# Performance work log

Hardware: AMD Instinct MI355X
Metric: run time of the kernel (lower is better)

The kernel has to match this reference:

```python
import jax, jax.numpy as jnp
import numpy as np

B, S, D_MODEL, HEADS = 2, 2048, 1024, 16
HEAD_DIM = D_MODEL // HEADS
NEG = -1.0e9


def setup_inputs() -> dict:
    key = jax.random.key(0)
    ks = jax.random.split(key, 7)
    query = jax.random.normal(ks[0], (B, S, D_MODEL), dtype=jnp.float32)
    k_in = jax.random.normal(ks[1], (B, S, D_MODEL), dtype=jnp.float32)
    value = jax.random.normal(ks[2], (B, S, D_MODEL), dtype=jnp.float32)
    # nn.Linear(d_model, d_model, bias=False) weights, torch layout [out, in]
    sc = 1.0 / np.sqrt(D_MODEL)
    Wq = jax.random.uniform(ks[3], (D_MODEL, D_MODEL), jnp.float32, -sc, sc)
    Wk = jax.random.uniform(ks[4], (D_MODEL, D_MODEL), jnp.float32, -sc, sc)
    Wv = jax.random.uniform(ks[5], (D_MODEL, D_MODEL), jnp.float32, -sc, sc)
    Wo = jax.random.uniform(ks[6], (D_MODEL, D_MODEL), jnp.float32, -sc, sc)
    # causal mask: 1 where attention allowed, 0 where masked
    mask = jnp.tril(jnp.ones((S, S), dtype=jnp.int32))[None, None]
    freqs_complex_form = jnp.zeros((1,), dtype=jnp.float32)  # unused by the module
    return {"query": query, "key": k_in, "value": value,
            "freqs_complex_form": freqs_complex_form, "mask": mask,
            "Wq": Wq, "Wk": Wk, "Wv": Wv, "Wo": Wo}


def reference(query, key, value, freqs_complex_form, mask, Wq, Wk, Wv, Wo):
    # QKV projections (torch Linear: y = x @ W.T)
    q = query @ Wq.T
    k = key @ Wk.T
    v = value @ Wv.T
    # [B, S, D] -> [B, H, S, Dh]
    q = q.reshape(B, S, HEADS, HEAD_DIM).transpose(0, 2, 1, 3)
    k = k.reshape(B, S, HEADS, HEAD_DIM).transpose(0, 2, 1, 3)
    v = v.reshape(B, S, HEADS, HEAD_DIM).transpose(0, 2, 1, 3)
    # scores [B, H, S, S]
    att = jnp.einsum('bhqd,bhkd->bhqk', q, k) / jnp.sqrt(jnp.float32(HEAD_DIM))
    att = jnp.where(mask == 0, NEG, att)
    att = jax.nn.softmax(att, axis=-1)
    # dropout is identity in eval / deterministic reference
    out = jnp.einsum('bhqk,bhkd->bhqd', att, v)
    out = out.transpose(0, 2, 1, 3).reshape(B, S, D_MODEL)
    return out @ Wo.T
```

## Files before the change

### kernel.cpp

```cpp
#include <hip/hip_runtime.h>

#define DM   1024
#define SEQ  2048
#define BATCH 2
#define NH   16
#define DHEAD 64
#define MTOT (BATCH*SEQ)
#define KVB  64

typedef _Float16 half_t;
typedef _Float16 half8 __attribute__((ext_vector_type(8)));
typedef float    floatx4 __attribute__((ext_vector_type(4)));

#define SCALE2 0.18033688f

__device__ __forceinline__ float fast_exp2(float x) {
  float r;
  asm volatile("v_exp_f32 %0, %1" : "=v"(r) : "v"(x));
  return r;
}

__device__ __forceinline__ void gload_lds16(const half_t* g, half_t* l) {
  __builtin_amdgcn_global_load_lds(
      (const __attribute__((address_space(1))) void*)g,
      (__attribute__((address_space(3))) void*)l, 16, 0, 0);
}

__global__ __launch_bounds__(256) void cvt_all(const float* __restrict__ q, const float* __restrict__ k,
                                               const float* __restrict__ v, const float* __restrict__ wq,
                                               const float* __restrict__ wk, const float* __restrict__ wv,
                                               const float* __restrict__ wo,
                                               half_t* __restrict__ dq, half_t* __restrict__ dk,
                                               half_t* __restrict__ dv, half_t* __restrict__ dwq,
                                               half_t* __restrict__ dwk, half_t* __restrict__ dwv,
                                               half_t* __restrict__ dwo) {
  const int y = blockIdx.y;
  const float* s; half_t* d; int n8;
  const int En8 = MTOT * DM / 8, Wn8 = DM * DM / 8;
  switch (y) {
    case 0: s = q;  d = dq;  n8 = En8; break;
    case 1: s = k;  d = dk;  n8 = En8; break;
    case 2: s = v;  d = dv;  n8 = En8; break;
    case 3: s = wq; d = dwq; n8 = Wn8; break;
    case 4: s = wk; d = dwk; n8 = Wn8; break;
    case 5: s = wv; d = dwv; n8 = Wn8; break;
    default: s = wo; d = dwo; n8 = Wn8; break;
  }
  int i = blockIdx.x * 256 + threadIdx.x;
  if (i >= n8) return;
  const float4* sp = reinterpret_cast<const float4*>(s);
  float4 u = sp[(size_t)i * 2], w = sp[(size_t)i * 2 + 1];
  half8 h;
  h[0] = (half_t)u.x; h[1] = (half_t)u.y; h[2] = (half_t)u.z; h[3] = (half_t)u.w;
  h[4] = (half_t)w.x; h[5] = (half_t)w.y; h[6] = (half_t)w.z; h[7] = (half_t)w.w;
  *reinterpret_cast<half8*>(d + (size_t)i * 8) = h;
}


#define GEMM_BODY(Ag, Bg, ...)                                                  \
  __shared__ half_t As[2][128 * 32];                                            \
  __shared__ half_t Bs[2][128 * 32];                                            \
  const int tid = threadIdx.x, lane = tid & 63, w = tid >> 6;                   \
  const int lr = lane & 15, lg = lane >> 4;                                     \
  const int swz = (flat & 7) * 32 + (flat >> 3);                                \
  const int m0 = (swz & 31) * 128, n0 = (swz >> 5) * 128;                       \
  const int wm = (w >> 1) * 64, wn = (w & 1) * 64;                              \
  floatx4 acc[4][4] = {};                                                       \
   \
  _Pragma("unroll")                                                             \
  for (int j = 0; j < 2; j++) {                                                 \
    int id = tid + j * 256;                                                     \
    gload_lds16(Ag + (size_t)(m0 + (id >> 2)) * DM + (id & 3) * 8,              \
                &As[0][id * 8]);                                                \
    gload_lds16(Bg + (size_t)(n0 + (id >> 2)) * DM + (id & 3) * 8,              \
                &Bs[0][id * 8]);                                                \
  }                                                                             \
  __syncthreads();                                                              \
  int buf = 0;                                                                  \
  _Pragma("unroll 1")                                                           \
  for (int t = 0; t < 31; t++) {                                                \
    const int k0 = (t + 1) * 32;                                                \
    _Pragma("unroll")                                                           \
    for (int j = 0; j < 2; j++) {                                               \
      int id = tid + j * 256;                                                   \
      gload_lds16(Ag + (size_t)(m0 + (id >> 2)) * DM + k0 + (id & 3) * 8,       \
                  &As[buf ^ 1][id * 8]);                                        \
      gload_lds16(Bg + (size_t)(n0 + (id >> 2)) * DM + k0 + (id & 3) * 8,       \
                  &Bs[buf ^ 1][id * 8]);                                        \
    }                                                                           \
    {                                                                           \
      half8 a[4], b[4];                                                         \
      _Pragma("unroll")                                                         \
      for (int i = 0; i < 4; i++)                                               \
        a[i] = *reinterpret_cast<half8*>(&As[buf][(wm + i * 16 + lr) * 32 + lg * 8]); \
      _Pragma("unroll")                                                         \
      for (int j = 0; j < 4; j++)                                               \
        b[j] = *reinterpret_cast<half8*>(&Bs[buf][(wn + j * 16 + lr) * 32 + lg * 8]); \
      _Pragma("unroll")                                                         \
      for (int i = 0; i < 4; i++)                                               \
        _Pragma("unroll")                                                       \
        for (int j = 0; j < 4; j++)                                             \
          acc[i][j] = __builtin_amdgcn_mfma_f32_16x16x32_f16(a[i], b[j],        \
                                                             acc[i][j], 0, 0, 0); \
    }                                                                           \
    __syncthreads();                                                            \
    buf ^= 1;                                                                   \
  }                                                                             \
  {                                                                             \
    half8 a[4], b[4];                                                           \
    _Pragma("unroll")                                                           \
    for (int i = 0; i < 4; i++)                                                 \
      a[i] = *reinterpret_cast<half8*>(&As[buf][(wm + i * 16 + lr) * 32 + lg * 8]); \
    _Pragma("unroll")                                                           \
    for (int j = 0; j < 4; j++)                                                 \
      b[j] = *reinterpret_cast<half8*>(&Bs[buf][(wn + j * 16 + lr) * 32 + lg * 8]); \
    _Pragma("unroll")                                                           \
    for (int i = 0; i < 4; i++)                                                 \
      _Pragma("unroll")                                                         \
      for (int j = 0; j < 4; j++)                                               \
        acc[i][j] = __builtin_amdgcn_mfma_f32_16x16x32_f16(a[i], b[j],          \
                                                           acc[i][j], 0, 0, 0); \
  }                                                                             \
  _Pragma("unroll")                                                             \
  for (int i = 0; i < 4; i++)                                                   \
    _Pragma("unroll")                                                           \
    for (int j = 0; j < 4; j++)                                                 \
      _Pragma("unroll")                                                         \
      for (int r = 0; r < 4; r++) {                                             \
        int m = m0 + wm + i * 16 + lg * 4 + r;                                  \
        int n = n0 + wn + j * 16 + lr;                                          \
        float v = acc[i][j][r];                                                 \
        __VA_ARGS__                                                             \
      }

__global__ __launch_bounds__(256) void gemm_qkv(const half_t* __restrict__ Xq,
                                                const half_t* __restrict__ Xk,
                                                const half_t* __restrict__ Xv,
                                                const half_t* __restrict__ Wq,
                                                const half_t* __restrict__ Wk,
                                                const half_t* __restrict__ Wv,
                                                half_t* __restrict__ Qb,
                                                half_t* __restrict__ Kb,
                                                half_t* __restrict__ Vb) {
  const int which = blockIdx.x >> 8;
  const int flat = blockIdx.x & 255;
  const half_t* Ag = (which == 0) ? Xq : (which == 1) ? Xk : Xv;
  const half_t* Bg = (which == 0) ? Wq : (which == 1) ? Wk : Wv;
  half_t* Cg       = (which == 0) ? Qb : (which == 1) ? Kb : Vb;
  const float esc  = (which == 0) ? SCALE2 : 1.0f;
  GEMM_BODY(Ag, Bg,
    int b_ = m >> 11;
    int s_ = m & 2047;
    int h_ = n >> 6;
    int d_ = n & 63;
    Cg[(((size_t)b_ * NH + h_) * SEQ + s_) * DHEAD + d_] = (half_t)(v * esc);)
}

__global__ __launch_bounds__(256) void gemm_o(const half_t* __restrict__ Ag,
                                              const half_t* __restrict__ Bg,
                                              float* __restrict__ Cg) {
  const int flat = blockIdx.x;
  GEMM_BODY(Ag, Bg, Cg[(size_t)m * DM + n] = v;)
}

__global__ __launch_bounds__(256) void attn_fwd(const half_t* __restrict__ Q,
                                                const half_t* __restrict__ K,
                                                const half_t* __restrict__ V,
                                                half_t* __restrict__ O) {
  __shared__ half_t Ks[64][72];
  __shared__ half_t Vt[80][72];
  __shared__ half_t Ps[4][16][72];
  const int tid = threadIdx.x, lane = tid & 63, w = tid >> 6;
  const int lr = lane & 15, lg = lane >> 4;

  const int flat = blockIdx.x;
  const int xcd = flat & 7, idx = flat >> 3;
  const int qblk = 31 - (idx >> 2);
  const int combo = xcd * 4 + (idx & 3);
  const int h = combo & 15, b = combo >> 4;

  const size_t bh = ((size_t)b * NH + h) * SEQ * DHEAD;
  const int q0 = qblk * 64 + w * 16;
  const int nt = qblk + 1;

  for (int i2 = tid; i2 < 16 * 72; i2 += 256) {
    int d = i2 / 72, kv = i2 % 72;
    Vt[64 + d][kv] = (d == 0) ? (half_t)1.0f : (half_t)0.0f;
  }

  half8 qf[2];
#pragma unroll
  for (int ks = 0; ks < 2; ks++)
    qf[ks] = *reinterpret_cast<const half8*>(
        Q + bh + (size_t)(q0 + lr) * DHEAD + ks * 32 + lg * 8);

  floatx4 accO[5] = {};

  half8 kr[2], vr[2];
#define LOADT(t)                                                              \
  {                                                                           \
    const int kvb2 = (t) * KVB;                                               \
    _Pragma("unroll")                                                         \
    for (int it = 0; it < 2; it++) {                                          \
      int c = tid + it * 256;                                                 \
      kr[it] = *reinterpret_cast<const half8*>(                               \
          K + bh + (size_t)(kvb2 + (c >> 3)) * DHEAD + (c & 7) * 8);          \
      vr[it] = *reinterpret_cast<const half8*>(                               \
          V + bh + (size_t)(kvb2 + (c & 63)) * DHEAD + (c >> 6) * 8);         \
    }                                                                         \
  }
#define WRITET()                                                              \
  {                                                                           \
    _Pragma("unroll")                                                         \
    for (int it = 0; it < 2; it++) {                                          \
      int c = tid + it * 256;                                                 \
      *reinterpret_cast<half8*>(&Ks[c >> 3][(c & 7) * 8]) = kr[it];           \
      int vrow = c & 63, vcol = (c >> 6) * 8;                                 \
      _Pragma("unroll")                                                       \
      for (int e = 0; e < 8; e++) Vt[vcol + e][vrow] = vr[it][e];             \
    }                                                                         \
  }

  LOADT(0);
  WRITET();
  __syncthreads();

#pragma unroll 1
  for (int t = 0; t < nt; t++) {
    const int kvbase = t * KVB;
    if (t + 1 < nt) LOADT(t + 1);
    const bool need_mask = (t == qblk);
    {
      floatx4 s[4];
#pragma unroll
      for (int jt = 0; jt < 4; jt++) {
        floatx4 a0 = {};
#pragma unroll
        for (int ks = 0; ks < 2; ks++) {
          half8 bk = *reinterpret_cast<half8*>(&Ks[jt * 16 + lr][ks * 32 + lg * 8]);
          a0 = __builtin_amdgcn_mfma_f32_16x16x32_f16(qf[ks], bk, a0, 0, 0, 0);
        }
        s[jt] = a0;
      }
#pragma unroll
      for (int r = 0; r < 4; r++) {
        const int q = q0 + lg * 4 + r;
#pragma unroll
        for (int jt = 0; jt < 4; jt++) {
          float pp = fast_exp2(s[jt][r]);
          if (need_mask) { int kv = kvbase + jt * 16 + lr; if (kv > q) pp = 0.f; }
          Ps[w][lg * 4 + r][jt * 16 + lr] = (half_t)pp;
        }
      }
#pragma unroll
      for (int j = 0; j < 5; j++) {
#pragma unroll
        for (int ks = 0; ks < 2; ks++) {
          half8 ap = *reinterpret_cast<half8*>(&Ps[w][lr][ks * 32 + lg * 8]);
          half8 bv = *reinterpret_cast<half8*>(&Vt[j * 16 + lr][ks * 32 + lg * 8]);
          accO[j] = __builtin_amdgcn_mfma_f32_16x16x32_f16(ap, bv, accO[j], 0, 0, 0);
        }
      }
    }
    if (t + 1 < nt) {
      __syncthreads();
      WRITET();
      __syncthreads();
    }
  }

#pragma unroll
  for (int r = 0; r < 4; r++) {
    float lsum = __shfl(accO[4][r], lane & 48);
    float inv = 1.0f / lsum;
    int q = q0 + lg * 4 + r;
#pragma unroll
    for (int j = 0; j < 4; j++) {
      float v = accO[j][r] * inv;
      O[((size_t)b * SEQ + q) * DM + h * DHEAD + j * 16 + lr] = (half_t)v;
    }
  }
#undef LOADT
#undef WRITET
}

extern "C" void kernel_launch(void* const* d_in, const int* in_sizes, int n_in,
                              void* d_out, int out_size, void* d_ws, size_t ws_size,
                              hipStream_t stream) {
  const float* q_in = (const float*)d_in[0];
  const float* k_in = (const float*)d_in[1];
  const float* v_in = (const float*)d_in[2];
  const float* Wq   = (const float*)d_in[5];
  const float* Wk   = (const float*)d_in[6];
  const float* Wv   = (const float*)d_in[7];
  const float* Wo   = (const float*)d_in[8];

  const size_t E = (size_t)MTOT * DM;
  const size_t W = (size_t)DM * DM;
  half_t* ws  = (half_t*)d_ws;
  half_t* Xq  = ws;
  half_t* Xk  = ws + E;
  half_t* Xv  = ws + 2 * E;
  half_t* Wqh = ws + 3 * E;
  half_t* Wkh = Wqh + W;
  half_t* Wvh = Wkh + W;
  half_t* Woh = Wvh + W;
  half_t* Qb  = ws + 4 * E;
  half_t* Kb  = ws + 5 * E;
  half_t* Vb  = ws + 6 * E;
  half_t* Ab  = Xq;
  if (ws_size < 7 * E * sizeof(half_t)) return;

  cvt_all<<<dim3(2048, 7), 256, 0, stream>>>(q_in, k_in, v_in, Wq, Wk, Wv, Wo,
                                             Xq, Xk, Xv, Wqh, Wkh, Wvh, Woh);
  gemm_qkv<<<768, 256, 0, stream>>>(Xq, Xk, Xv, Wqh, Wkh, Wvh, Qb, Kb, Vb);
  attn_fwd<<<1024, 256, 0, stream>>>(Qb, Kb, Vb, Ab);
  gemm_o<<<256, 256, 0, stream>>>(Ab, Woh, (float*)d_out);
}
```

Measured before the change: 141.1 us.

## Split attention KV range in two with a combine pass, narrow output GEMM tiles

The attention kernel now launches twice as many blocks. Each block handles half of the causal KV tiles for its query block and writes an unnormalized partial output plus a row-sum. A new combine kernel adds the two partials, normalizes them, and writes the head-interleaved activation. This is meant to improve load balance and occupancy across the triangular causal work, at the cost of an extra kernel and extra global traffic for the partial buffers. The output projection GEMM also switches to 128x64 tiles with 512 blocks, giving more parallelism on the smaller GEMM. The shared GEMM macro is replaced by explicit per-kernel code.

```diff
diff --git a/kernel.cpp b/kernel.cpp
--- a/kernel.cpp
+++ b/kernel.cpp
@@ -7,6 +7,8 @@
 #define DHEAD 64
 #define MTOT (BATCH*SEQ)
 #define KVB  64
+#define EOFF ((size_t)MTOT * DM)
+#define NROW (BATCH * NH * SEQ)
 
 typedef _Float16 half_t;
 typedef _Float16 half8 __attribute__((ext_vector_type(8)));
@@ -56,83 +58,6 @@
   *reinterpret_cast<half8*>(d + (size_t)i * 8) = h;
 }
 
-
-#define GEMM_BODY(Ag, Bg, ...)                                                  \
-  __shared__ half_t As[2][128 * 32];                                            \
-  __shared__ half_t Bs[2][128 * 32];                                            \
-  const int tid = threadIdx.x, lane = tid & 63, w = tid >> 6;                   \
-  const int lr = lane & 15, lg = lane >> 4;                                     \
-  const int swz = (flat & 7) * 32 + (flat >> 3);                                \
-  const int m0 = (swz & 31) * 128, n0 = (swz >> 5) * 128;                       \
-  const int wm = (w >> 1) * 64, wn = (w & 1) * 64;                              \
-  floatx4 acc[4][4] = {};                                                       \
-   \
-  _Pragma("unroll")                                                             \
-  for (int j = 0; j < 2; j++) {                                                 \
-    int id = tid + j * 256;                                                     \
-    gload_lds16(Ag + (size_t)(m0 + (id >> 2)) * DM + (id & 3) * 8,              \
-                &As[0][id * 8]);                                                \
-    gload_lds16(Bg + (size_t)(n0 + (id >> 2)) * DM + (id & 3) * 8,              \
-                &Bs[0][id * 8]);                                                \
-  }                                                                             \
-  __syncthreads();                                                              \
-  int buf = 0;                                                                  \
-  _Pragma("unroll 1")                                                           \
-  for (int t = 0; t < 31; t++) {                                                \
-    const int k0 = (t + 1) * 32;                                                \
-    _Pragma("unroll")                                                           \
-    for (int j = 0; j < 2; j++) {                                               \
-      int id = tid + j * 256;                                                   \
-      gload_lds16(Ag + (size_t)(m0 + (id >> 2)) * DM + k0 + (id & 3) * 8,       \
-                  &As[buf ^ 1][id * 8]);                                        \
-      gload_lds16(Bg + (size_t)(n0 + (id >> 2)) * DM + k0 + (id & 3) * 8,       \
-                  &Bs[buf ^ 1][id * 8]);                                        \
-    }                                                                           \
-    {                                                                           \
-      half8 a[4], b[4];                                                         \
-      _Pragma("unroll")                                                         \
-      for (int i = 0; i < 4; i++)                                               \
-        a[i] = *reinterpret_cast<half8*>(&As[buf][(wm + i * 16 + lr) * 32 + lg * 8]); \
-      _Pragma("unroll")                                                         \
-      for (int j = 0; j < 4; j++)                                               \
-        b[j] = *reinterpret_cast<half8*>(&Bs[buf][(wn + j * 16 + lr) * 32 + lg * 8]); \
-      _Pragma("unroll")                                                         \
-      for (int i = 0; i < 4; i++)                                               \
-        _Pragma("unroll")                                                       \
-        for (int j = 0; j < 4; j++)                                             \
-          acc[i][j] = __builtin_amdgcn_mfma_f32_16x16x32_f16(a[i], b[j],        \
-                                                             acc[i][j], 0, 0, 0); \
-    }                                                                           \
-    __syncthreads();                                                            \
-    buf ^= 1;                                                                   \
-  }                                                                             \
-  {                                                                             \
-    half8 a[4], b[4];                                                           \
-    _Pragma("unroll")                                                           \
-    for (int i = 0; i < 4; i++)                                                 \
-      a[i] = *reinterpret_cast<half8*>(&As[buf][(wm + i * 16 + lr) * 32 + lg * 8]); \
-    _Pragma("unroll")                                                           \
-    for (int j = 0; j < 4; j++)                                                 \
-      b[j] = *reinterpret_cast<half8*>(&Bs[buf][(wn + j * 16 + lr) * 32 + lg * 8]); \
-    _Pragma("unroll")                                                           \
-    for (int i = 0; i < 4; i++)                                                 \
-      _Pragma("unroll")                                                         \
-      for (int j = 0; j < 4; j++)                                               \
-        acc[i][j] = __builtin_amdgcn_mfma_f32_16x16x32_f16(a[i], b[j],          \
-                                                           acc[i][j], 0, 0, 0); \
-  }                                                                             \
-  _Pragma("unroll")                                                             \
-  for (int i = 0; i < 4; i++)                                                   \
-    _Pragma("unroll")                                                           \
-    for (int j = 0; j < 4; j++)                                                 \
-      _Pragma("unroll")                                                         \
-      for (int r = 0; r < 4; r++) {                                             \
-        int m = m0 + wm + i * 16 + lg * 4 + r;                                  \
-        int n = n0 + wn + j * 16 + lr;                                          \
-        float v = acc[i][j][r];                                                 \
-        __VA_ARGS__                                                             \
-      }
-
 __global__ __launch_bounds__(256) void gemm_qkv(const half_t* __restrict__ Xq,
                                                 const half_t* __restrict__ Xk,
                                                 const half_t* __restrict__ Xv,
@@ -142,31 +67,147 @@
                                                 half_t* __restrict__ Qb,
                                                 half_t* __restrict__ Kb,
                                                 half_t* __restrict__ Vb) {
+  __shared__ half_t As[2][128 * 32];
+  __shared__ half_t Bs[2][128 * 32];
   const int which = blockIdx.x >> 8;
   const int flat = blockIdx.x & 255;
   const half_t* Ag = (which == 0) ? Xq : (which == 1) ? Xk : Xv;
   const half_t* Bg = (which == 0) ? Wq : (which == 1) ? Wk : Wv;
   half_t* Cg       = (which == 0) ? Qb : (which == 1) ? Kb : Vb;
   const float esc  = (which == 0) ? SCALE2 : 1.0f;
-  GEMM_BODY(Ag, Bg,
-    int b_ = m >> 11;
-    int s_ = m & 2047;
-    int h_ = n >> 6;
-    int d_ = n & 63;
-    Cg[(((size_t)b_ * NH + h_) * SEQ + s_) * DHEAD + d_] = (half_t)(v * esc);)
+
+  const int tid = threadIdx.x, lane = tid & 63, w = tid >> 6;
+  const int lr = lane & 15, lg = lane >> 4;
+  const int swz = (flat & 7) * 32 + (flat >> 3);
+  const int m0 = (swz & 31) * 128, n0 = (swz >> 5) * 128;
+  const int wm = (w >> 1) * 64, wn = (w & 1) * 64;
+  floatx4 acc[4][4] = {};
+
+#define STAGE_QKV(BUF, K0)                                                    \
+  {                                                                           \
+    _Pragma("unroll")                                                         \
+    for (int j = 0; j < 2; j++) {                                             \
+      int id = tid + j * 256;                                                 \
+      gload_lds16(Ag + (size_t)(m0 + (id >> 2)) * DM + (K0) + (id & 3) * 8,   \
+                  &As[BUF][id * 8]);                                          \
+      gload_lds16(Bg + (size_t)(n0 + (id >> 2)) * DM + (K0) + (id & 3) * 8,   \
+                  &Bs[BUF][id * 8]);                                          \
+    }                                                                         \
+  }
+#define COMP_QKV(BUF)                                                         \
+  {                                                                           \
+    half8 a[4], b[4];                                                         \
+    _Pragma("unroll")                                                         \
+    for (int i = 0; i < 4; i++)                                               \
+      a[i] = *reinterpret_cast<half8*>(&As[BUF][(wm + i * 16 + lr) * 32 + lg * 8]); \
+    _Pragma("unroll")                                                         \
+    for (int j = 0; j < 4; j++)                                               \
+      b[j] = *reinterpret_cast<half8*>(&Bs[BUF][(wn + j * 16 + lr) * 32 + lg * 8]); \
+    _Pragma("unroll")                                                         \
+    for (int i = 0; i < 4; i++)                                               \
+      _Pragma("unroll")                                                       \
+      for (int j = 0; j < 4; j++)                                             \
+        acc[i][j] = __builtin_amdgcn_mfma_f32_16x16x32_f16(a[i], b[j], acc[i][j], 0, 0, 0); \
+  }
+
+  STAGE_QKV(0, 0);
+  __syncthreads();
+  int buf = 0;
+#pragma unroll 1
+  for (int t = 0; t < 31; t++) {
+    STAGE_QKV(buf ^ 1, (t + 1) * 32);
+    COMP_QKV(buf);
+    __syncthreads();
+    buf ^= 1;
+  }
+  COMP_QKV(buf);
+
+#pragma unroll
+  for (int i = 0; i < 4; i++)
+#pragma unroll
+    for (int j = 0; j < 4; j++)
+#pragma unroll
+      for (int r = 0; r < 4; r++) {
+        int m = m0 + wm + i * 16 + lg * 4 + r;
+        int n = n0 + wn + j * 16 + lr;
+        int b_ = m >> 11, s_ = m & 2047, h_ = n >> 6, d_ = n & 63;
+        Cg[(((size_t)b_ * NH + h_) * SEQ + s_) * DHEAD + d_] = (half_t)(acc[i][j][r] * esc);
+      }
+#undef STAGE_QKV
+#undef COMP_QKV
 }
 
 __global__ __launch_bounds__(256) void gemm_o(const half_t* __restrict__ Ag,
                                               const half_t* __restrict__ Bg,
                                               float* __restrict__ Cg) {
+  __shared__ half_t As[2][128 * 32];
+  __shared__ half_t Bs[2][64 * 32];
+  const int tid = threadIdx.x, lane = tid & 63, w = tid >> 6;
+  const int lr = lane & 15, lg = lane >> 4;
   const int flat = blockIdx.x;
-  GEMM_BODY(Ag, Bg, Cg[(size_t)m * DM + n] = v;)
+  const int swz = (flat & 7) * 64 + (flat >> 3);
+  const int m0 = (swz & 31) * 128, n0 = (swz >> 5) * 64;
+  const int wm = (w >> 1) * 64, wn = (w & 1) * 32;
+  floatx4 acc[4][2] = {};
+
+#define STAGE_O(BUF, K0)                                                      \
+  {                                                                           \
+    _Pragma("unroll")                                                         \
+    for (int j = 0; j < 2; j++) {                                             \
+      int id = tid + j * 256;                                                 \
+      gload_lds16(Ag + (size_t)(m0 + (id >> 2)) * DM + (K0) + (id & 3) * 8,   \
+                  &As[BUF][id * 8]);                                          \
+    }                                                                         \
+    gload_lds16(Bg + (size_t)(n0 + (tid >> 2)) * DM + (K0) + (tid & 3) * 8,   \
+                &Bs[BUF][tid * 8]);                                           \
+  }
+#define COMP_O(BUF)                                                           \
+  {                                                                           \
+    half8 a[4], b[2];                                                         \
+    _Pragma("unroll")                                                         \
+    for (int i = 0; i < 4; i++)                                               \
+      a[i] = *reinterpret_cast<half8*>(&As[BUF][(wm + i * 16 + lr) * 32 + lg * 8]); \
+    _Pragma("unroll")                                                         \
+    for (int j = 0; j < 2; j++)                                               \
+      b[j] = *reinterpret_cast<half8*>(&Bs[BUF][(wn + j * 16 + lr) * 32 + lg * 8]); \
+    _Pragma("unroll")                                                         \
+    for (int i = 0; i < 4; i++)                                               \
+      _Pragma("unroll")                                                       \
+      for (int j = 0; j < 2; j++)                                             \
+        acc[i][j] = __builtin_amdgcn_mfma_f32_16x16x32_f16(a[i], b[j], acc[i][j], 0, 0, 0); \
+  }
+
+  STAGE_O(0, 0);
+  __syncthreads();
+  int buf = 0;
+#pragma unroll 1
+  for (int t = 0; t < 31; t++) {
+    STAGE_O(buf ^ 1, (t + 1) * 32);
+    COMP_O(buf);
+    __syncthreads();
+    buf ^= 1;
+  }
+  COMP_O(buf);
+
+#pragma unroll
+  for (int i = 0; i < 4; i++)
+#pragma unroll
+    for (int j = 0; j < 2; j++)
+#pragma unroll
+      for (int r = 0; r < 4; r++) {
+        int m = m0 + wm + i * 16 + lg * 4 + r;
+        int n = n0 + wn + j * 16 + lr;
+        Cg[(size_t)m * DM + n] = acc[i][j][r];
+      }
+#undef STAGE_O
+#undef COMP_O
 }
 
 __global__ __launch_bounds__(256) void attn_fwd(const half_t* __restrict__ Q,
                                                 const half_t* __restrict__ K,
                                                 const half_t* __restrict__ V,
-                                                half_t* __restrict__ O) {
+                                                half_t* __restrict__ P,
+                                                float* __restrict__ L) {
   __shared__ half_t Ks[64][72];
   __shared__ half_t Vt[80][72];
   __shared__ half_t Ps[4][16][72];
@@ -175,13 +216,18 @@
 
   const int flat = blockIdx.x;
   const int xcd = flat & 7, idx = flat >> 3;
-  const int qblk = 31 - (idx >> 2);
-  const int combo = xcd * 4 + (idx & 3);
+  const int qblk = 31 - (idx >> 3);
+  const int sub = idx & 7;
+  const int combo = xcd * 4 + (sub >> 1);
+  const int split = sub & 1;
   const int h = combo & 15, b = combo >> 4;
 
   const size_t bh = ((size_t)b * NH + h) * SEQ * DHEAD;
   const int q0 = qblk * 64 + w * 16;
   const int nt = qblk + 1;
+  const int h0 = (nt + 1) >> 1;
+  const int t0 = split ? h0 : 0;
+  const int t1 = split ? nt : h0;
 
   for (int i2 = tid; i2 < 16 * 72; i2 += 256) {
     int d = i2 / 72, kv = i2 % 72;
@@ -221,67 +267,90 @@
     }                                                                         \
   }
 
-  LOADT(0);
-  WRITET();
-  __syncthreads();
+  if (t0 < t1) {
+    LOADT(t0);
+    WRITET();
+    __syncthreads();
 
 #pragma unroll 1
-  for (int t = 0; t < nt; t++) {
-    const int kvbase = t * KVB;
-    if (t + 1 < nt) LOADT(t + 1);
-    const bool need_mask = (t == qblk);
-    {
-      floatx4 s[4];
-#pragma unroll
-      for (int jt = 0; jt < 4; jt++) {
-        floatx4 a0 = {};
-#pragma unroll
-        for (int ks = 0; ks < 2; ks++) {
-          half8 bk = *reinterpret_cast<half8*>(&Ks[jt * 16 + lr][ks * 32 + lg * 8]);
-          a0 = __builtin_amdgcn_mfma_f32_16x16x32_f16(qf[ks], bk, a0, 0, 0, 0);
+    for (int t = t0; t < t1; t++) {
+      const int kvbase = t * KVB;
+      if (t + 1 < t1) LOADT(t + 1);
+      const bool need_mask = (t == qblk);
+      {
+        floatx4 s[4];
+#pragma unroll
+        for (int jt = 0; jt < 4; jt++) {
+          floatx4 a0 = {};
+#pragma unroll
+          for (int ks = 0; ks < 2; ks++) {
+            half8 bk = *reinterpret_cast<half8*>(&Ks[jt * 16 + lr][ks * 32 + lg * 8]);
+            a0 = __builtin_amdgcn_mfma_f32_16x16x32_f16(qf[ks], bk, a0, 0, 0, 0);
+          }
+          s[jt] = a0;
         }
-        s[jt] = a0;
-      }
-#pragma unroll
-      for (int r = 0; r < 4; r++) {
-        const int q = q0 + lg * 4 + r;
-#pragma unroll
-        for (int jt = 0; jt < 4; jt++) {
-          float pp = fast_exp2(s[jt][r]);
-          if (need_mask) { int kv = kvbase + jt * 16 + lr; if (kv > q) pp = 0.f; }
-          Ps[w][lg * 4 + r][jt * 16 + lr] = (half_t)pp;
+#pragma unroll
+        for (int r = 0; r < 4; r++) {
+          const int q = q0 + lg * 4 + r;
+#pragma unroll
+          for (int jt = 0; jt < 4; jt++) {
+            float pp = fast_exp2(s[jt][r]);
+            if (need_mask) { int kv = kvbase + jt * 16 + lr; if (kv > q) pp = 0.f; }
+            Ps[w][lg * 4 + r][jt * 16 + lr] = (half_t)pp;
+          }
+        }
+        half8 ap0 = *reinterpret_cast<half8*>(&Ps[w][lr][lg * 8]);
+        half8 ap1 = *reinterpret_cast<half8*>(&Ps[w][lr][32 + lg * 8]);
+#pragma unroll
+        for (int j = 0; j < 5; j++) {
+          half8 bv0 = *reinterpret_cast<half8*>(&Vt[j * 16 + lr][lg * 8]);
+          half8 bv1 = *reinterpret_cast<half8*>(&Vt[j * 16 + lr][32 + lg * 8]);
+          accO[j] = __builtin_amdgcn_mfma_f32_16x16x32_f16(ap0, bv0, accO[j], 0, 0, 0);
+          accO[j] = __builtin_amdgcn_mfma_f32_16x16x32_f16(ap1, bv1, accO[j], 0, 0, 0);
         }
       }
-#pragma unroll
-      for (int j = 0; j < 5; j++) {
-#pragma unroll
-        for (int ks = 0; ks < 2; ks++) {
-          half8 ap = *reinterpret_cast<half8*>(&Ps[w][lr][ks * 32 + lg * 8]);
-          half8 bv = *reinterpret_cast<half8*>(&Vt[j * 16 + lr][ks * 32 + lg * 8]);
-          accO[j] = __builtin_amdgcn_mfma_f32_16x16x32_f16(ap, bv, accO[j], 0, 0, 0);
-        }
+      if (t + 1 < t1) {
+        __syncthreads();
+        WRITET();
+        __syncthreads();
       }
     }
-    if (t + 1 < nt) {
-      __syncthreads();
-      WRITET();
-      __syncthreads();
-    }
-  }
-
+  }
+
+  half_t* Pw = P + (size_t)split * EOFF;
+  float*  Lw = L + (size_t)split * NROW;
 #pragma unroll
   for (int r = 0; r < 4; r++) {
-    float lsum = __shfl(accO[4][r], lane & 48);
-    float inv = 1.0f / lsum;
     int q = q0 + lg * 4 + r;
-#pragma unroll
-    for (int j = 0; j < 4; j++) {
-      float v = accO[j][r] * inv;
-      O[((size_t)b * SEQ + q) * DM + h * DHEAD + j * 16 + lr] = (half_t)v;
-    }
+    size_t rowbase = bh + (size_t)q * DHEAD;
+#pragma unroll
+    for (int j = 0; j < 4; j++)
+      Pw[rowbase + j * 16 + lr] = (half_t)accO[j][r];
+    if (lr == 0)
+      Lw[((size_t)b * NH + h) * SEQ + q] = accO[4][r];
   }
 #undef LOADT
 #undef WRITET
+}
+
+__global__ __launch_bounds__(256) void attn_combine(const half_t* __restrict__ P,
+                                                    const float* __restrict__ L,
+                                                    half_t* __restrict__ Ab) {
+  size_t i = (size_t)blockIdx.x * 256 + threadIdx.x;
+  half8 p0 = *reinterpret_cast<const half8*>(P + i * 8);
+  half8 p1 = *reinterpret_cast<const half8*>(P + EOFF + i * 8);
+  size_t row = i >> 3;
+  float l = L[row] + L[NROW + row];
+  float inv = 1.0f / l;
+  int s_ = (int)(row % SEQ);
+  int h_ = (int)((row / SEQ) % NH);
+  int b_ = (int)(row / ((size_t)SEQ * NH));
+  int d0 = (int)(i & 7) * 8;
+  half8 o;
+#pragma unroll
+  for (int e = 0; e < 8; e++)
+    o[e] = (half_t)(((float)p0[e] + (float)p1[e]) * inv);
+  *reinterpret_cast<half8*>(Ab + ((size_t)b_ * SEQ + s_) * DM + h_ * DHEAD + d0) = o;
 }
 
 extern "C" void kernel_launch(void* const* d_in, const int* in_sizes, int n_in,
@@ -295,7 +364,7 @@
   const float* Wv   = (const float*)d_in[7];
   const float* Wo   = (const float*)d_in[8];
 
-  const size_t E = (size_t)MTOT * DM;
+  const size_t E = EOFF;
   const size_t W = (size_t)DM * DM;
   half_t* ws  = (half_t*)d_ws;
   half_t* Xq  = ws;
@@ -309,11 +378,14 @@
   half_t* Kb  = ws + 5 * E;
   half_t* Vb  = ws + 6 * E;
   half_t* Ab  = Xq;
+  half_t* Pp  = Xk;
+  float*  Lp  = (float*)Wqh;
   if (ws_size < 7 * E * sizeof(half_t)) return;
 
   cvt_all<<<dim3(2048, 7), 256, 0, stream>>>(q_in, k_in, v_in, Wq, Wk, Wv, Wo,
                                              Xq, Xk, Xv, Wqh, Wkh, Wvh, Woh);
   gemm_qkv<<<768, 256, 0, stream>>>(Xq, Xk, Xv, Wqh, Wkh, Wvh, Qb, Kb, Vb);
-  attn_fwd<<<1024, 256, 0, stream>>>(Qb, Kb, Vb, Ab);
-  gemm_o<<<256, 256, 0, stream>>>(Ab, Woh, (float*)d_out);
-}
+  attn_fwd<<<2048, 256, 0, stream>>>(Qb, Kb, Vb, Pp, Lp);
+  attn_combine<<<2048, 256, 0, stream>>>(Pp, Lp, Ab);
+  gemm_o<<<512, 256, 0, stream>>>(Ab, Woh, (float*)d_out);
+}
```

Result: faster. 136.2 us (-3.5%).
